# Kernel tuning notes

Measured on AMD Instinct MI355X. Metric: run time of the kernel, lower is better.

## Reference

```python
import jax, jax.numpy as jnp
import numpy as np

H = 768  # bert-base hidden size; match MLP width = 2*H = 1536


def setup_inputs() -> dict:
    key = jax.random.key(0)
    ks = jax.random.split(key, 6)
    B, S = 2, 256
    std = 0.02  # TruncatedNormal(stddev=initializer_range)
    return {
        "hidden": jax.random.normal(ks[0], (B, S, H), dtype=jnp.float32),
        "w_start": jax.random.normal(ks[1], (H, 1), dtype=jnp.float32) * std,
        "b_start": jnp.zeros((1,), jnp.float32),
        "w_end": jax.random.normal(ks[2], (H, 1), dtype=jnp.float32) * std,
        "b_end": jnp.zeros((1,), jnp.float32),
        "w1": jax.random.normal(ks[3], (2 * H, 2 * H), dtype=jnp.float32) * std,
        "b1": jnp.zeros((2 * H,), jnp.float32),
        "w2": jax.random.normal(ks[4], (2 * H, 1), dtype=jnp.float32) * std,
        "b2": jnp.zeros((1,), jnp.float32),
    }


def reference(hidden, w_start, b_start, w_end, b_end, w1, b1, w2, b2):
    # hidden: [B, S, H] = BERT sequence output (dropout disabled at inference)
    start_logits = hidden @ w_start + b_start  # [B, S, 1]
    end_logits = hidden @ w_end + b_end        # [B, S, 1]

    # Pairwise span features: concat(row_i, col_j) along last dim, fed to dense1.
    # concat([row, col]) @ w1 == row @ w1[:H] + col @ w1[H:], so we split w1 and
    # broadcast-add instead of materializing the [B,S,S,2H] concat tile.
    row_proj = hidden @ w1[:H]   # [B, S, 2H] (start-token contribution)
    col_proj = hidden @ w1[H:]   # [B, S, 2H] (end-token contribution)
    pre = row_proj[:, :, None, :] + col_proj[:, None, :, :] + b1  # [B, S, S, 2H]
    act = jax.nn.gelu(pre, approximate=False)  # keras 'gelu' is exact
    match_logits = act @ w2 + b2  # [B, S, S, 1]
    return start_logits, end_logits, match_logits
```

## Files before the change

kernel.cpp:

```cpp
#include <hip/hip_runtime.h>
#include <stdint.h>

typedef __attribute__((ext_vector_type(8))) __bf16 bf16x8;
typedef __attribute__((ext_vector_type(4))) float  floatx4;
typedef __attribute__((ext_vector_type(4))) unsigned int uint4v;
typedef __attribute__((ext_vector_type(2))) unsigned int uint2v;
typedef __attribute__((ext_vector_type(4))) float  float4v;
typedef __attribute__((ext_vector_type(2))) float  float2v;

__device__ __forceinline__ unsigned short f2bf(float f) {
  union { float f; unsigned int u; } x; x.f = f;
  unsigned int r = x.u + 0x7fffu + ((x.u >> 16) & 1u);
  return (unsigned short)(r >> 16);
}

__global__ __launch_bounds__(256) void logits_init_kernel(
    const float* __restrict__ hidden, const float* __restrict__ w_start,
    const float* __restrict__ b_start, const float* __restrict__ w_end,
    const float* __restrict__ b_end, const float* __restrict__ b2,
    float* __restrict__ out) {
  if (blockIdx.x >= 32) {
    float v = b2[0];
    int idx = ((blockIdx.x - 32) * 256 + threadIdx.x) * 4;
    *(float4v*)(out + 1024 + idx) = float4v{v, v, v, v};
    return;
  }
  const int tid  = threadIdx.x;
  const int lane = tid & 63;
  const int wv   = tid >> 6;
  const int wg   = blockIdx.x * 4 + wv;

  float wsv[12], wev[12];
#pragma unroll
  for (int t = 0; t < 12; ++t) {
    wsv[t] = w_start[lane + 64 * t];
    wev[t] = w_end[lane + 64 * t];
  }
  const float bs = b_start[0];
  const float be = b_end[0];

#pragma unroll
  for (int r = 0; r < 4; ++r) {
    int row = wg * 4 + r;
    const float* h = hidden + (size_t)row * 768;
    float ps = 0.f, pe = 0.f;
#pragma unroll
    for (int t = 0; t < 12; ++t) {
      float hv = h[lane + 64 * t];
      ps += hv * wsv[t];
      pe += hv * wev[t];
    }
#pragma unroll
    for (int off = 32; off >= 1; off >>= 1) {
      ps += __shfl_xor(ps, off, 64);
      pe += __shfl_xor(pe, off, 64);
    }
    if (lane == 0) { out[row] = ps + bs; out[512 + row] = pe + be; }
  }
}

__global__ __launch_bounds__(256) void proj_kernel(
    const float* __restrict__ hidden, const float* __restrict__ w1,
    const float* __restrict__ b1, unsigned short* __restrict__ wsR,
    unsigned short* __restrict__ wsC) {
  __shared__ short As[4 * 32 * 8];
  __shared__ short Bs[4 * 64 * 8];

  const int tid  = threadIdx.x;
  const int lane = tid & 63;
  const int wave = tid >> 6;
  const int wr = wave >> 1, wc = wave & 1;
  const int m0 = blockIdx.y * 32;
  const int n0g = blockIdx.x * 64;
  const bool isR = (n0g < 1536);
  const int kbase = isR ? 0 : 768;
  const int n0 = isR ? n0g : (n0g - 1536);
  const int q = lane >> 4, l15 = lane & 15;

  floatx4 acc0 = {}, acc1 = {};

  const int a_row = tid >> 3;
  const int a_s   = tid & 7;
  const int b_n   = tid & 63;
  const int b_kg  = tid >> 6;

  const float* hrow = hidden + (size_t)(m0 + a_row) * 768 + a_s * 4;
  const float* bcol = w1 + (size_t)(kbase + b_kg * 8) * 1536 + n0 + b_n;

  float4v hv = *(const float4v*)(hrow);
  float bv[8];
#pragma unroll
  for (int a = 0; a < 8; ++a) bv[a] = bcol[(size_t)a * 1536];

  const int aq = a_s >> 1;
  const int aj = (a_s & 1) * 4;

  for (int ko = 0; ko < 768; ko += 32) {
    uint2v au;
    au[0] = (unsigned int)f2bf(hv[0]) | ((unsigned int)f2bf(hv[1]) << 16);
    au[1] = (unsigned int)f2bf(hv[2]) | ((unsigned int)f2bf(hv[3]) << 16);
    *(uint2v*)(&As[(aq * 32 + a_row) * 8 + aj]) = au;
    uint4v pv;
#pragma unroll
    for (int a = 0; a < 4; ++a) {
      unsigned int lo = f2bf(bv[2 * a]);
      unsigned int hi = f2bf(bv[2 * a + 1]);
      pv[a] = lo | (hi << 16);
    }
    *(uint4v*)(&Bs[(b_kg * 64 + b_n) * 8]) = pv;
    __syncthreads();

    if (ko + 32 < 768) {
      hv = *(const float4v*)(hrow + ko + 32);
      const float* bp = bcol + (size_t)(ko + 32) * 1536;
#pragma unroll
      for (int a = 0; a < 8; ++a) bv[a] = bp[(size_t)a * 1536];
    }

    bf16x8 af  = *(const bf16x8*)(&As[(q * 32 + 16 * wr + l15) * 8]);
    bf16x8 bg0 = *(const bf16x8*)(&Bs[(q * 64 + 32 * wc + l15) * 8]);
    bf16x8 bg1 = *(const bf16x8*)(&Bs[(q * 64 + 32 * wc + 16 + l15) * 8]);
    acc0 = __builtin_amdgcn_mfma_f32_16x16x32_bf16(af, bg0, acc0, 0, 0, 0);
    acc1 = __builtin_amdgcn_mfma_f32_16x16x32_bf16(af, bg1, acc1, 0, 0, 0);
    __syncthreads();
  }

  unsigned short* outp = isR ? wsR : wsC;
#pragma unroll
  for (int ni = 0; ni < 2; ++ni) {
    const floatx4& ac = ni ? acc1 : acc0;
    int col = n0 + 32 * wc + 16 * ni + l15;
    float bias = isR ? b1[col] : 0.0f;
#pragma unroll
    for (int r = 0; r < 4; ++r) {
      int rowg = m0 + 16 * wr + q * 4 + r;
      outp[(size_t)rowg * 1536 + col] = f2bf(ac[r] + bias);
    }
  }
}

__device__ __forceinline__ float2v gelu2_acc(float2v x, float2v wv, float2v acc) {
  constexpr float C0 = 0.39103831f;
  constexpr float C1 = -0.05415410f;
  constexpr float C2 = 0.00461682f;
  constexpr float C3 = -1.51033e-4f;
  float2v xc;
  xc[0] = __builtin_amdgcn_fmed3f(x[0], -3.5f, 3.5f);
  xc[1] = __builtin_amdgcn_fmed3f(x[1], -3.5f, 3.5f);
  float2v u = xc * xc;
  float2v p = __builtin_elementwise_fma(u,
      __builtin_elementwise_fma(u,
          __builtin_elementwise_fma(u, float2v{C3, C3}, float2v{C2, C2}),
          float2v{C1, C1}),
      float2v{C0, C0});
  float2v t = __builtin_elementwise_fma(xc, p, float2v{0.5f, 0.5f});
  float2v g = x * t;
  return __builtin_elementwise_fma(g, wv, acc);
}

__global__ __launch_bounds__(256) void match_kernel(
    const unsigned short* __restrict__ wsR,
    const unsigned short* __restrict__ wsC,
    const float* __restrict__ w2,
    float* __restrict__ outm) {
  __shared__ float Rs[16 * 260];
  __shared__ float Cs[16 * 260];
  __shared__ float Ws[256];

  const int tid = threadIdx.x;
  const int jt = blockIdx.x, it = blockIdx.y;
  const int bz = blockIdx.z >> 1, kh = blockIdx.z & 1;
  const int i = tid >> 4, j = tid & 15;

  float2v a01 = {0.f, 0.f};
  float2v a23 = {0.f, 0.f};

  const int srow = tid >> 4;
  const int scc  = tid & 15;

  for (int kc = 0; kc < 3; ++kc) {
    const int Kb = kh * 768 + kc * 256;
    {
      const unsigned short* rg = wsR + (size_t)(bz * 256 + it * 16 + srow) * 1536 + Kb + scc * 16;
      const unsigned short* cg = wsC + (size_t)(bz * 256 + jt * 16 + srow) * 1536 + Kb + scc * 16;
      uint4v rv0 = *(const uint4v*)rg;
      uint4v rv1 = *(const uint4v*)(rg + 8);
      uint4v cv0 = *(const uint4v*)cg;
      uint4v cv1 = *(const uint4v*)(cg + 8);
      float* rd = &Rs[srow * 260 + scc * 16];
      float* cd = &Cs[srow * 260 + scc * 16];
      float4v t0, t1, t2, t3;
#pragma unroll
      for (int a = 0; a < 2; ++a) {
        union { unsigned int u; float f; } lo, hi;
        lo.u = rv0[2*a] << 16;   hi.u = rv0[2*a] & 0xffff0000u;
        t0[2*a] = lo.f; t0[2*a+1] = hi.f;
        lo.u = rv0[2*a+1] << 16; hi.u = rv0[2*a+1] & 0xffff0000u;
        t1[2*a] = lo.f; t1[2*a+1] = hi.f;
        lo.u = rv1[2*a] << 16;   hi.u = rv1[2*a] & 0xffff0000u;
        t2[2*a] = lo.f; t2[2*a+1] = hi.f;
        lo.u = rv1[2*a+1] << 16; hi.u = rv1[2*a+1] & 0xffff0000u;
        t3[2*a] = lo.f; t3[2*a+1] = hi.f;
      }
      float4v r0 = float4v{t0[0], t0[1], t1[0], t1[1]};
      float4v r1 = float4v{t0[2], t0[3], t1[2], t1[3]};
      float4v r2 = float4v{t2[0], t2[1], t3[0], t3[1]};
      float4v r3 = float4v{t2[2], t2[3], t3[2], t3[3]};
      *(float4v*)rd        = r0;
      *(float4v*)(rd + 4)  = r1;
      *(float4v*)(rd + 8)  = r2;
      *(float4v*)(rd + 12) = r3;
#pragma unroll
      for (int a = 0; a < 2; ++a) {
        union { unsigned int u; float f; } lo, hi;
        lo.u = cv0[2*a] << 16;   hi.u = cv0[2*a] & 0xffff0000u;
        t0[2*a] = lo.f; t0[2*a+1] = hi.f;
        lo.u = cv0[2*a+1] << 16; hi.u = cv0[2*a+1] & 0xffff0000u;
        t1[2*a] = lo.f; t1[2*a+1] = hi.f;
        lo.u = cv1[2*a] << 16;   hi.u = cv1[2*a] & 0xffff0000u;
        t2[2*a] = lo.f; t2[2*a+1] = hi.f;
        lo.u = cv1[2*a+1] << 16; hi.u = cv1[2*a+1] & 0xffff0000u;
        t3[2*a] = lo.f; t3[2*a+1] = hi.f;
      }
      float4v c0 = float4v{t0[0], t0[1], t1[0], t1[1]};
      float4v c1 = float4v{t0[2], t0[3], t1[2], t1[3]};
      float4v c2 = float4v{t2[0], t2[1], t3[0], t3[1]};
      float4v c3 = float4v{t2[2], t2[3], t3[2], t3[3]};
      *(float4v*)cd        = c0;
      *(float4v*)(cd + 4)  = c1;
      *(float4v*)(cd + 8)  = c2;
      *(float4v*)(cd + 12) = c3;
      Ws[tid] = w2[Kb + tid];
    }
    __syncthreads();

    const float* rp = &Rs[i * 260];
    const float* cp = &Cs[j * 260];
#pragma unroll 2
    for (int k = 0; k < 256; k += 8) {
      float4v r0 = *(const float4v*)(rp + k);
      float4v r1 = *(const float4v*)(rp + k + 4);
      float4v c0 = *(const float4v*)(cp + k);
      float4v c1 = *(const float4v*)(cp + k + 4);
      float4v w0 = *(const float4v*)(&Ws[k]);
      float4v w1v = *(const float4v*)(&Ws[k + 4]);
      {
        float2v rA = {r0[0], r0[1]}, cA = {c0[0], c0[1]};
        a01 = gelu2_acc(rA + cA, float2v{w0[0], w0[1]}, a01);
        float2v rB = {r0[2], r0[3]}, cB = {c0[2], c0[3]};
        a23 = gelu2_acc(rB + cB, float2v{w0[2], w0[3]}, a23);
      }
      {
        float2v rC = {r1[0], r1[1]}, cC = {c1[0], c1[1]};
        a01 = gelu2_acc(rC + cC, float2v{w1v[0], w1v[1]}, a01);
        float2v rD = {r1[2], r1[3]}, cD = {c1[2], c1[3]};
        a23 = gelu2_acc(rD + cD, float2v{w1v[2], w1v[3]}, a23);
      }
    }
    __syncthreads();
  }

  float acc = (a01[0] + a01[1]) + (a23[0] + a23[1]);
  size_t idx = ((size_t)bz * 256 + it * 16 + i) * 256 + (jt * 16 + j);
  unsafeAtomicAdd(&outm[idx], acc);
}

extern "C" void kernel_launch(void* const* d_in, const int* in_sizes, int n_in,
                              void* d_out, int out_size, void* d_ws, size_t ws_size,
                              hipStream_t stream) {
  const float* hidden  = (const float*)d_in[0];
  const float* w_start = (const float*)d_in[1];
  const float* b_start = (const float*)d_in[2];
  const float* w_end   = (const float*)d_in[3];
  const float* b_end   = (const float*)d_in[4];
  const float* w1      = (const float*)d_in[5];
  const float* b1      = (const float*)d_in[6];
  const float* w2      = (const float*)d_in[7];
  const float* b2      = (const float*)d_in[8];

  float* out = (float*)d_out;
  char* ws = (char*)d_ws;
  unsigned short* wsR = (unsigned short*)(ws);
  unsigned short* wsC = (unsigned short*)(ws + 1572864);

  logits_init_kernel<<<dim3(160), dim3(256), 0, stream>>>(
      hidden, w_start, b_start, w_end, b_end, b2, out);
  proj_kernel<<<dim3(48, 16), dim3(256), 0, stream>>>(hidden, w1, b1, wsR, wsC);
  match_kernel<<<dim3(16, 16, 4), dim3(256), 0, stream>>>(wsR, wsC, w2, out + 1024);
}
```

Before: 131.5 us.

## Register-block match kernel 2x4 outputs per thread with 4-way K split

Each thread in the match kernel now computes a 2x4 block of (i,j) outputs instead of one, so each row/column value loaded from LDS is reused across several GELU evaluations. The block tile becomes 32x64 with a 128-wide K chunk, and the K dimension is split four ways across the grid instead of two. This cuts LDS read traffic per GELU and puts more independent accumulators in flight. In exchange it raises register pressure, doubles the atomic adds into the output, and shrinks the grid to 256 blocks.

```diff
diff --git a/kernel.cpp b/kernel.cpp
--- a/kernel.cpp
+++ b/kernel.cpp
@@ -158,111 +158,137 @@
   return __builtin_elementwise_fma(g, wv, acc);
 }
 
+__device__ __forceinline__ void g8(float2v& acc, float4v r0, float4v r1,
+                                   float4v c0, float4v c1,
+                                   float4v w0, float4v w1) {
+  acc = gelu2_acc(float2v{r0[0], r0[1]} + float2v{c0[0], c0[1]},
+                  float2v{w0[0], w0[1]}, acc);
+  acc = gelu2_acc(float2v{r0[2], r0[3]} + float2v{c0[2], c0[3]},
+                  float2v{w0[2], w0[3]}, acc);
+  acc = gelu2_acc(float2v{r1[0], r1[1]} + float2v{c1[0], c1[1]},
+                  float2v{w1[0], w1[1]}, acc);
+  acc = gelu2_acc(float2v{r1[2], r1[3]} + float2v{c1[2], c1[3]},
+                  float2v{w1[2], w1[3]}, acc);
+}
+
+__device__ __forceinline__ void cvt8(uint4v v, float4v& lo4, float4v& hi4) {
+  union { unsigned int u; float f; } t;
+  float4v L, H;
+  t.u = v[0] << 16;          L[0] = t.f;
+  t.u = v[0] & 0xffff0000u;  L[1] = t.f;
+  t.u = v[1] << 16;          L[2] = t.f;
+  t.u = v[1] & 0xffff0000u;  L[3] = t.f;
+  t.u = v[2] << 16;          H[0] = t.f;
+  t.u = v[2] & 0xffff0000u;  H[1] = t.f;
+  t.u = v[3] << 16;          H[2] = t.f;
+  t.u = v[3] & 0xffff0000u;  H[3] = t.f;
+  lo4 = L; hi4 = H;
+}
+
 __global__ __launch_bounds__(256) void match_kernel(
     const unsigned short* __restrict__ wsR,
     const unsigned short* __restrict__ wsC,
     const float* __restrict__ w2,
     float* __restrict__ outm) {
-  __shared__ float Rs[16 * 260];
-  __shared__ float Cs[16 * 260];
-  __shared__ float Ws[256];
+  __shared__ float Rs[32 * 132];
+  __shared__ float Cs[64 * 132];
+  __shared__ float Ws[128];
 
   const int tid = threadIdx.x;
-  const int jt = blockIdx.x, it = blockIdx.y;
-  const int bz = blockIdx.z >> 1, kh = blockIdx.z & 1;
-  const int i = tid >> 4, j = tid & 15;
-
-  float2v a01 = {0.f, 0.f};
-  float2v a23 = {0.f, 0.f};
+  const int jt = blockIdx.x;
+  const int it = blockIdx.y;
+  const int bz = blockIdx.z >> 2;
+  const int kh = blockIdx.z & 3;
+
+  const int rg  = tid >> 4;
+  const int cgl = tid & 15;
+
+  float2v accA0 = {}, accA1 = {}, accA2 = {}, accA3 = {};
+  float2v accB0 = {}, accB1 = {}, accB2 = {}, accB3 = {};
 
   const int srow = tid >> 4;
-  const int scc  = tid & 15;
+  const int sseg = tid & 15;
+
+  const float* rp0 = &Rs[(2 * rg + 0) * 132];
+  const float* rp1 = &Rs[(2 * rg + 1) * 132];
+  const float* cp0 = &Cs[(cgl +  0) * 132];
+  const float* cp1 = &Cs[(cgl + 16) * 132];
+  const float* cp2 = &Cs[(cgl + 32) * 132];
+  const float* cp3 = &Cs[(cgl + 48) * 132];
 
   for (int kc = 0; kc < 3; ++kc) {
-    const int Kb = kh * 768 + kc * 256;
-    {
-      const unsigned short* rg = wsR + (size_t)(bz * 256 + it * 16 + srow) * 1536 + Kb + scc * 16;
-      const unsigned short* cg = wsC + (size_t)(bz * 256 + jt * 16 + srow) * 1536 + Kb + scc * 16;
-      uint4v rv0 = *(const uint4v*)rg;
-      uint4v rv1 = *(const uint4v*)(rg + 8);
-      uint4v cv0 = *(const uint4v*)cg;
-      uint4v cv1 = *(const uint4v*)(cg + 8);
-      float* rd = &Rs[srow * 260 + scc * 16];
-      float* cd = &Cs[srow * 260 + scc * 16];
-      float4v t0, t1, t2, t3;
-#pragma unroll
-      for (int a = 0; a < 2; ++a) {
-        union { unsigned int u; float f; } lo, hi;
-        lo.u = rv0[2*a] << 16;   hi.u = rv0[2*a] & 0xffff0000u;
-        t0[2*a] = lo.f; t0[2*a+1] = hi.f;
-        lo.u = rv0[2*a+1] << 16; hi.u = rv0[2*a+1] & 0xffff0000u;
-        t1[2*a] = lo.f; t1[2*a+1] = hi.f;
-        lo.u = rv1[2*a] << 16;   hi.u = rv1[2*a] & 0xffff0000u;
-        t2[2*a] = lo.f; t2[2*a+1] = hi.f;
-        lo.u = rv1[2*a+1] << 16; hi.u = rv1[2*a+1] & 0xffff0000u;
-        t3[2*a] = lo.f; t3[2*a+1] = hi.f;
-      }
-      float4v r0 = float4v{t0[0], t0[1], t1[0], t1[1]};
-      float4v r1 = float4v{t0[2], t0[3], t1[2], t1[3]};
-      float4v r2 = float4v{t2[0], t2[1], t3[0], t3[1]};
-      float4v r3 = float4v{t2[2], t2[3], t3[2], t3[3]};
-      *(float4v*)rd        = r0;
-      *(float4v*)(rd + 4)  = r1;
-      *(float4v*)(rd + 8)  = r2;
-      *(float4v*)(rd + 12) = r3;
-#pragma unroll
-      for (int a = 0; a < 2; ++a) {
-        union { unsigned int u; float f; } lo, hi;
-        lo.u = cv0[2*a] << 16;   hi.u = cv0[2*a] & 0xffff0000u;
-        t0[2*a] = lo.f; t0[2*a+1] = hi.f;
-        lo.u = cv0[2*a+1] << 16; hi.u = cv0[2*a+1] & 0xffff0000u;
-        t1[2*a] = lo.f; t1[2*a+1] = hi.f;
-        lo.u = cv1[2*a] << 16;   hi.u = cv1[2*a] & 0xffff0000u;
-        t2[2*a] = lo.f; t2[2*a+1] = hi.f;
-        lo.u = cv1[2*a+1] << 16; hi.u = cv1[2*a+1] & 0xffff0000u;
-        t3[2*a] = lo.f; t3[2*a+1] = hi.f;
-      }
-      float4v c0 = float4v{t0[0], t0[1], t1[0], t1[1]};
-      float4v c1 = float4v{t0[2], t0[3], t1[2], t1[3]};
-      float4v c2 = float4v{t2[0], t2[1], t3[0], t3[1]};
-      float4v c3 = float4v{t2[2], t2[3], t3[2], t3[3]};
-      *(float4v*)cd        = c0;
-      *(float4v*)(cd + 4)  = c1;
-      *(float4v*)(cd + 8)  = c2;
-      *(float4v*)(cd + 12) = c3;
-      Ws[tid] = w2[Kb + tid];
-    }
+    const int Kb = kh * 384 + kc * 128;
+#pragma unroll
+    for (int a = 0; a < 2; ++a) {
+      int row = srow + 16 * a;
+      const unsigned short* g =
+          wsR + (size_t)(bz * 256 + it * 32 + row) * 1536 + Kb + sseg * 8;
+      uint4v v = *(const uint4v*)g;
+      float4v lo, hi; cvt8(v, lo, hi);
+      float* d = &Rs[row * 132 + sseg * 8];
+      *(float4v*)d = lo;
+      *(float4v*)(d + 4) = hi;
+    }
+#pragma unroll
+    for (int a = 0; a < 4; ++a) {
+      int row = srow + 16 * a;
+      const unsigned short* g =
+          wsC + (size_t)(bz * 256 + jt * 64 + row) * 1536 + Kb + sseg * 8;
+      uint4v v = *(const uint4v*)g;
+      float4v lo, hi; cvt8(v, lo, hi);
+      float* d = &Cs[row * 132 + sseg * 8];
+      *(float4v*)d = lo;
+      *(float4v*)(d + 4) = hi;
+    }
+    if (tid < 128) Ws[tid] = w2[Kb + tid];
     __syncthreads();
 
-    const float* rp = &Rs[i * 260];
-    const float* cp = &Cs[j * 260];
 #pragma unroll 2
-    for (int k = 0; k < 256; k += 8) {
-      float4v r0 = *(const float4v*)(rp + k);
-      float4v r1 = *(const float4v*)(rp + k + 4);
-      float4v c0 = *(const float4v*)(cp + k);
-      float4v c1 = *(const float4v*)(cp + k + 4);
-      float4v w0 = *(const float4v*)(&Ws[k]);
-      float4v w1v = *(const float4v*)(&Ws[k + 4]);
+    for (int k = 0; k < 128; k += 8) {
+      float4v ra0 = *(const float4v*)(rp0 + k);
+      float4v ra1 = *(const float4v*)(rp0 + k + 4);
+      float4v rb0 = *(const float4v*)(rp1 + k);
+      float4v rb1 = *(const float4v*)(rp1 + k + 4);
+      float4v w0  = *(const float4v*)(&Ws[k]);
+      float4v w1  = *(const float4v*)(&Ws[k + 4]);
       {
-        float2v rA = {r0[0], r0[1]}, cA = {c0[0], c0[1]};
-        a01 = gelu2_acc(rA + cA, float2v{w0[0], w0[1]}, a01);
-        float2v rB = {r0[2], r0[3]}, cB = {c0[2], c0[3]};
-        a23 = gelu2_acc(rB + cB, float2v{w0[2], w0[3]}, a23);
+        float4v c0 = *(const float4v*)(cp0 + k);
+        float4v c1 = *(const float4v*)(cp0 + k + 4);
+        g8(accA0, ra0, ra1, c0, c1, w0, w1);
+        g8(accB0, rb0, rb1, c0, c1, w0, w1);
       }
       {
-        float2v rC = {r1[0], r1[1]}, cC = {c1[0], c1[1]};
-        a01 = gelu2_acc(rC + cC, float2v{w1v[0], w1v[1]}, a01);
-        float2v rD = {r1[2], r1[3]}, cD = {c1[2], c1[3]};
-        a23 = gelu2_acc(rD + cD, float2v{w1v[2], w1v[3]}, a23);
+        float4v c0 = *(const float4v*)(cp1 + k);
+        float4v c1 = *(const float4v*)(cp1 + k + 4);
+        g8(accA1, ra0, ra1, c0, c1, w0, w1);
+        g8(accB1, rb0, rb1, c0, c1, w0, w1);
       }
+      {
+        float4v c0 = *(const float4v*)(cp2 + k);
+        float4v c1 = *(const float4v*)(cp2 + k + 4);
+        g8(accA2, ra0, ra1, c0, c1, w0, w1);
+        g8(accB2, rb0, rb1, c0, c1, w0, w1);
+      }
+      {
+        float4v c0 = *(const float4v*)(cp3 + k);
+        float4v c1 = *(const float4v*)(cp3 + k + 4);
+        g8(accA3, ra0, ra1, c0, c1, w0, w1);
+        g8(accB3, rb0, rb1, c0, c1, w0, w1);
+      }
     }
     __syncthreads();
   }
 
-  float acc = (a01[0] + a01[1]) + (a23[0] + a23[1]);
-  size_t idx = ((size_t)bz * 256 + it * 16 + i) * 256 + (jt * 16 + j);
-  unsafeAtomicAdd(&outm[idx], acc);
+  const size_t rowA = (size_t)(bz * 256 + it * 32 + 2 * rg);
+  const size_t base = rowA * 256 + jt * 64 + cgl;
+  unsafeAtomicAdd(&outm[base +  0], accA0[0] + accA0[1]);
+  unsafeAtomicAdd(&outm[base + 16], accA1[0] + accA1[1]);
+  unsafeAtomicAdd(&outm[base + 32], accA2[0] + accA2[1]);
+  unsafeAtomicAdd(&outm[base + 48], accA3[0] + accA3[1]);
+  unsafeAtomicAdd(&outm[base + 256 +  0], accB0[0] + accB0[1]);
+  unsafeAtomicAdd(&outm[base + 256 + 16], accB1[0] + accB1[1]);
+  unsafeAtomicAdd(&outm[base + 256 + 32], accB2[0] + accB2[1]);
+  unsafeAtomicAdd(&outm[base + 256 + 48], accB3[0] + accB3[1]);
 }
 
 extern "C" void kernel_launch(void* const* d_in, const int* in_sizes, int n_in,
@@ -286,5 +312,5 @@
   logits_init_kernel<<<dim3(160), dim3(256), 0, stream>>>(
       hidden, w_start, b_start, w_end, b_end, b2, out);
   proj_kernel<<<dim3(48, 16), dim3(256), 0, stream>>>(hidden, w1, b1, wsR, wsC);
-  match_kernel<<<dim3(16, 16, 4), dim3(256), 0, stream>>>(wsR, wsC, w2, out + 1024);
-}
+  match_kernel<<<dim3(4, 8, 8), dim3(256), 0, stream>>>(wsR, wsC, w2, out + 1024);
+}
```

Result: slower. 147.3 us (+12.0%).
